# Kernel optimization log

Measured on AMD Instinct MI355X. Metric: run time of the kernel, lower is better.

Reference implementation:

```python
import jax, jax.numpy as jnp
import numpy as np

TOKEN_SELF_ATTN_VALUE = -50000.0
EPS_NORM = 1e-12
EPS_SCATTER = 1e-5
COMMITMENT = 1e-4


def _l2norm(x):
    return x / jnp.maximum(jnp.linalg.norm(x, axis=-1, keepdims=True), EPS_NORM)


def _shift(x):
    # relative-position shift, faithful to the torch `shift` helper
    # x: [..., i, j] -> [..., i, j]
    *pre, i, j = x.shape
    x = jnp.concatenate([x, jnp.zeros((*pre, i, i), x.dtype)], axis=-1)  # [..., i, i+j]
    l = i + j - 1
    x = x.reshape(*pre, i * (i + j))
    pad = (-x.shape[-1]) % l
    x = jnp.concatenate([x, jnp.zeros((*pre, pad), x.dtype)], axis=-1)
    x = x.reshape(*pre, -1, l)
    return x[..., :i, i - 1:]


def setup_inputs() -> dict:
    key = jax.random.key(0)
    k1, k2, k3, k4 = jax.random.split(key, 4)
    b, h, t, d = 4, 8, 8192, 64
    c, wsz = 64, 128
    qk = jax.random.normal(k1, (b, h, t, d), jnp.float32)
    v = jax.random.normal(k2, (b, h, t, d), jnp.float32)
    means = jax.random.normal(k3, (h, c, d), jnp.float32)
    means = _l2norm(means)  # trained kmeans means are unit-normalized
    rel_w = jax.random.normal(k4, (wsz, h, d), jnp.float32) * 0.02
    return {"qk": qk, "v": v, "means": means, "rel_w": rel_w}


def reference(qk, v, means, rel_w):
    b, h, t, d = qk.shape
    c = means.shape[1]
    wsz = min(rel_w.shape[0], t)

    # ---- kmeans routing (eval path: no iterations, fixed means) ----
    k_routing = _l2norm(qk)                                   # [b,h,t,d]
    dists = jnp.einsum('bhld,hcd->bhlc', k_routing, means)    # cosine sims
    buckets = jnp.argmax(dists, axis=-1)                      # [b,h,t]
    # top-wsz tokens per cluster, sorted ascending (matches topk -> sort -> transpose)
    _, idx = jax.lax.top_k(jnp.swapaxes(dists, -1, -2), wsz)  # [b,h,c,wsz]
    indices = jnp.sort(idx, axis=-1).reshape(b, h, c * wsz)   # [b,h,c*wsz]

    # commitment loss against routed means (means is a non-trainable buffer)
    routed_means = means[jnp.arange(h)[None, :, None], buckets]  # [b,h,t,d]
    loss = jnp.mean((k_routing - routed_means) ** 2) * COMMITMENT

    # ---- gather routed windows ----
    qk_g = jnp.take_along_axis(qk, indices[..., None], axis=2).reshape(b, h, c, wsz, d)
    v_g = jnp.take_along_axis(v, indices[..., None], axis=2).reshape(b, h, c, wsz, d)
    q = qk_g
    k = _l2norm(qk_g)

    scale = d ** -0.5
    dots = jnp.einsum('bhnid,bhnjd->bhnij', q, k) * scale     # [b,h,c,wsz,wsz]
    rel = jnp.einsum('bhnid,jhd->bhnij', q, rel_w) * scale
    dots = dots + _shift(rel)

    # token cannot attend to itself within its window
    eye = jnp.eye(wsz, dtype=bool)
    dots = jnp.where(eye, TOKEN_SELF_ATTN_VALUE, dots)

    attn = jax.nn.softmax(dots, axis=-1)
    bo = jnp.einsum('bhnij,bhnjd->bhnid', attn, v_g).reshape(b, h, c * wsz, d)

    # ---- scatter-mean back to original token positions ----
    def scat(idx1, src1):  # idx1: [N], src1: [N,d]
        num = jnp.zeros((t, d), src1.dtype).at[idx1].add(src1)
        den = jnp.zeros((t, d), src1.dtype).at[idx1].add(jnp.ones_like(src1))
        return num / (den + EPS_SCATTER)

    out = jax.vmap(jax.vmap(scat))(indices, bo)               # [b,h,t,d]
    return out, loss
```

## Files before the change

kernel.cpp:

```cpp
#include <hip/hip_runtime.h>
#include <hip/hip_bf16.h>
#include <math.h>

#define NB 4
#define NH 8
#define TT 8192
#define DD 64
#define NC 64
#define WW 128
#define BHN 32
#define SCALE 0.125f
#define INVCAP 24
#define TPB 128

typedef __bf16  bf16x8 __attribute__((ext_vector_type(8)));
typedef float   f32x4  __attribute__((ext_vector_type(4)));
typedef double  f64x4  __attribute__((ext_vector_type(4)));
typedef unsigned long long u64;

#define MFMA(a, b, c) __builtin_amdgcn_mfma_f32_16x16x32_bf16((a), (b), (c), 0, 0, 0)

__device__ __forceinline__ u64 fixkey(double dv) {
    double k = (dv + 1.0) * 4611686018427387904.0;
    k = fmin(fmax(k, 0.0), 9223371487098961920.0);
    return (u64)k;
}

__global__ __launch_bounds__(256) void k_dists(
    const float* __restrict__ qk, const float* __restrict__ means,
    u64* __restrict__ keys, double* __restrict__ lossa)
{
    __shared__ float  qS[TPB * 66];
    __shared__ float  mS[NC * 65];
    __shared__ double invS[TPB];
    __shared__ double s2S[TPB];
    __shared__ double mn2[NC];
    __shared__ double red[4];

    const int bh  = blockIdx.x;
    const int h   = bh & 7;
    const int tid = threadIdx.x;
    const int t0  = blockIdx.y * TPB;

    {
        const float* mp = means + h * (NC * DD);
        for (int i = tid; i < NC * DD; i += 256)
            mS[(i >> 6) * 65 + (i & 63)] = mp[i];
    }
    {
        const float4* src = (const float4*)(qk + ((size_t)bh * TT + t0) * DD);
        for (int i = tid; i < TPB * DD / 4; i += 256) {
            const float4 v = src[i];
            float* dst = qS + (i >> 4) * 66 + (i & 15) * 4;
            *(float2*)(dst)     = make_float2(v.x, v.y);
            *(float2*)(dst + 2) = make_float2(v.z, v.w);
        }
    }
    __syncthreads();

    if (tid < NC) {
        double s = 0.0;
        const float* rp = mS + tid * 65;
        for (int d = 0; d < DD; d++) { const double m = (double)rp[d]; s = fma(m, m, s); }
        mn2[tid] = s;
    }
    if (tid < TPB) {
        double s = 0.0;
        const float* rp = qS + tid * 66;
#pragma unroll
        for (int d = 0; d < DD; d += 2) {
            const float2 f = *(const float2*)(rp + d);
            s = fma((double)f.x, (double)f.x, s);
            s = fma((double)f.y, (double)f.y, s);
        }
        const double inv = 1.0 / fmax(sqrt(s), 1e-12);
        invS[tid] = inv;
        s2S[tid]  = s * inv * inv;
    }
    __syncthreads();

    const int lane = tid & 63;
    const int wv   = tid >> 6;
    const int lo   = lane & 15;
    const int quad = lane >> 4;

    double lt_lane = 0.0;

#pragma unroll
    for (int tt = 0; tt < 2; tt++) {
        const int tloc = (wv * 2 + tt) * 16 + lo;
        double Bf[16];
#pragma unroll
        for (int s = 0; s < 16; s++)
            Bf[s] = (double)qS[tloc * 66 + quad + 4 * s];
        const double inv = invS[tloc];

        double rawmax = -1.0e300; int cbest = 0;
        u64* kout = keys + (size_t)bh * NC * TT + (t0 + tloc);

#pragma unroll
        for (int ct = 0; ct < 4; ct++) {
            f64x4 acc = (f64x4){0.0, 0.0, 0.0, 0.0};
#pragma unroll
            for (int s = 0; s < 16; s++) {
                const double Af = (double)mS[(ct * 16 + lo) * 65 + quad + 4 * s];
                acc = __builtin_amdgcn_mfma_f64_16x16x4f64(Af, Bf[s], acc, 0, 0, 0);
            }
#pragma unroll
            for (int r = 0; r < 4; r++) {
                const double raw = acc[r];
                const int c = ct * 16 + quad * 4 + r;
                if (raw > rawmax) { rawmax = raw; cbest = c; }
                kout[(size_t)c * TT] = fixkey(raw * inv);
            }
        }

#pragma unroll
        for (int off = 16; off < 64; off <<= 1) {
            const double ov = __shfl_xor(rawmax, off);
            const int    oc = __shfl_xor(cbest, off);
            if (ov > rawmax || (ov == rawmax && oc < cbest)) { rawmax = ov; cbest = oc; }
        }
        if (quad == 0)
            lt_lane += s2S[tloc] + mn2[cbest] - 2.0 * rawmax * inv;
    }

#pragma unroll
    for (int o = 32; o; o >>= 1) lt_lane += __shfl_xor(lt_lane, o);
    if (lane == 0) red[wv] = lt_lane;
    __syncthreads();
    if (tid == 0) atomicAdd(lossa, red[0] + red[1] + red[2] + red[3]);
}

__global__ __launch_bounds__(256) void k_topk(
    const u64* __restrict__ keys, int* __restrict__ indices,
    unsigned int* __restrict__ cnt, unsigned short* __restrict__ inv)
{
    __shared__ unsigned int hist[4][256];
    __shared__ int wsum[8];
    __shared__ int bc_bin, bc_rank, bc_cnt;

    const int bhc = blockIdx.x, tid = threadIdx.x;
    const int wv = tid >> 6, lane = tid & 63;
    const int bh = bhc >> 6;

    u64 key[32];
    {
        const ulonglong2* p = (const ulonglong2*)(keys + (size_t)bhc * TT + tid * 32);
#pragma unroll
        for (int i = 0; i < 16; i++) { ulonglong2 u = p[i]; key[2*i] = u.x; key[2*i+1] = u.y; }
    }

    u64 thr = 0;
    int need = 128, gshift = 55, prevShift = 0;
    unsigned int* hb = &hist[0][0];

    for (int level = 0; level < 8; level++) {
        const int shift = (level < 7) ? (55 - 8 * level) : 0;
        hb[tid] = 0; hb[tid + 256] = 0; hb[tid + 512] = 0; hb[tid + 768] = 0;
        __syncthreads();
        unsigned int* hw = hist[wv];
        if (level == 0) {
#pragma unroll
            for (int i = 0; i < 32; i++)
                atomicAdd(&hw[(unsigned int)(key[i] >> 55)], 1u);
        } else {
            const u64 pv = thr >> prevShift;
#pragma unroll
            for (int i = 0; i < 32; i++)
                if ((key[i] >> prevShift) == pv)
                    atomicAdd(&hw[(unsigned int)(key[i] >> shift) & 255u], 1u);
        }
        __syncthreads();

        const int b = 255 - tid;
        const int c = hist[0][b] + hist[1][b] + hist[2][b] + hist[3][b];
        int incl = c;
#pragma unroll
        for (int o = 1; o < 64; o <<= 1) {
            const int v = __shfl_up(incl, o);
            if (lane >= o) incl += v;
        }
        if (lane == 63) wsum[wv] = incl;
        __syncthreads();
        int above = incl - c;
        for (int wj = 0; wj < wv; wj++) above += wsum[wj];
        if (above < need && above + c >= need) {
            bc_bin = b; bc_rank = above; bc_cnt = c;
        }
        __syncthreads();
        thr |= ((u64)(unsigned int)bc_bin) << shift;
        need -= bc_rank;
        gshift = shift;
        prevShift = shift;
        if (bc_cnt == need || shift == 0) break;
    }

    const u64 tg = thr >> gshift;
    int cgt = 0, ceq = 0;
#pragma unroll
    for (int i = 0; i < 32; i++) {
        const u64 kg = key[i] >> gshift;
        cgt += (kg > tg) ? 1 : 0;
        ceq += (kg == tg) ? 1 : 0;
    }
    int ig = cgt, ie = ceq;
#pragma unroll
    for (int o = 1; o < 64; o <<= 1) {
        const int vg = __shfl_up(ig, o);
        const int ve = __shfl_up(ie, o);
        if (lane >= o) { ig += vg; ie += ve; }
    }
    if (lane == 63) { wsum[wv] = ig; wsum[4 + wv] = ie; }
    __syncthreads();
    int pgt = ig - cgt, peq = ie - ceq;
    for (int wj = 0; wj < wv; wj++) { pgt += wsum[wj]; peq += wsum[4 + wj]; }

    const int rneed = need;
    int* outp = indices + bhc * WW;
    unsigned int* cntb = cnt + (bh << 13);
    unsigned short* invb = inv + (((size_t)bh << 13) * INVCAP);
    const int cbase = (bhc & 63) * WW;
    int g = 0, e = 0;
#pragma unroll
    for (int i = 0; i < 32; i++) {
        const int tok = tid * 32 + i;
        const u64 kg = key[i] >> gshift;
        if (kg > tg) {
            const int tb = (peq + e < rneed) ? (peq + e) : rneed;
            const int wpos = pgt + g + tb;
            outp[wpos] = tok;
            const unsigned int pos = atomicAdd(&cntb[tok], 1u);
            if (pos < INVCAP) invb[(size_t)tok * INVCAP + pos] = (unsigned short)(cbase + wpos);
            g++;
        } else if (kg == tg) {
            if (peq + e < rneed) {
                const int wpos = pgt + g + peq + e;
                outp[wpos] = tok;
                const unsigned int pos = atomicAdd(&cntb[tok], 1u);
                if (pos < INVCAP) invb[(size_t)tok * INVCAP + pos] = (unsigned short)(cbase + wpos);
            }
            e++;
        }
    }
}

#define QS_ADDR(row, gi) (((row) << 6) + ((((gi) ^ ((row) & 7))) << 3))

__global__ __launch_bounds__(512) void k_attn(
    const float* __restrict__ qk, const float* __restrict__ vin,
    const float* __restrict__ rel_w, const int* __restrict__ indices,
    float* __restrict__ bo)
{
    __shared__ __attribute__((aligned(16))) __bf16 uv[64 * 136];
    __shared__ __attribute__((aligned(16))) __bf16 rs[128 * 136];
    __shared__ float invs[128];
    __shared__ int   idxs[128];

    const int tid  = threadIdx.x;
    const int lane = tid & 63;
    const int wv   = tid >> 6;
    const int lo   = lane & 15;
    const int quad = lane >> 4;
    const int rbase = wv * 16;

    const int bhc = blockIdx.x;
    const int bh  = bhc >> 6;
    const int h   = bh & 7;

    if (tid < 128) idxs[tid] = indices[bhc * WW + tid];
    __syncthreads();

    const int r  = tid >> 2;
    const int qp = tid & 3;
    const size_t rowoff = ((size_t)bh * TT + idxs[r]) * DD + qp * 16;
    float4 q0, q1, q2, q3, vreg[4];
    {
        const float4* qsrc = (const float4*)(qk + rowoff);
        q0 = qsrc[0]; q1 = qsrc[1]; q2 = qsrc[2]; q3 = qsrc[3];
        const float4* vsrc = (const float4*)(vin + rowoff);
        vreg[0] = vsrc[0]; vreg[1] = vsrc[1]; vreg[2] = vsrc[2]; vreg[3] = vsrc[3];
    }
    {
        float ssq = q0.x*q0.x + q0.y*q0.y + q0.z*q0.z + q0.w*q0.w
                  + q1.x*q1.x + q1.y*q1.y + q1.z*q1.z + q1.w*q1.w
                  + q2.x*q2.x + q2.y*q2.y + q2.z*q2.z + q2.w*q2.w
                  + q3.x*q3.x + q3.y*q3.y + q3.z*q3.z + q3.w*q3.w;
        ssq += __shfl_xor(ssq, 1);
        ssq += __shfl_xor(ssq, 2);
        if (qp == 0) invs[r] = 1.0f / fmaxf(sqrtf(ssq), 1e-12f);
        bf16x8 va, vb;
        va[0]=(__bf16)q0.x; va[1]=(__bf16)q0.y; va[2]=(__bf16)q0.z; va[3]=(__bf16)q0.w;
        va[4]=(__bf16)q1.x; va[5]=(__bf16)q1.y; va[6]=(__bf16)q1.z; va[7]=(__bf16)q1.w;
        vb[0]=(__bf16)q2.x; vb[1]=(__bf16)q2.y; vb[2]=(__bf16)q2.z; vb[3]=(__bf16)q2.w;
        vb[4]=(__bf16)q3.x; vb[5]=(__bf16)q3.y; vb[6]=(__bf16)q3.z; vb[7]=(__bf16)q3.w;
        *(bf16x8*)(uv + QS_ADDR(r, qp * 2))     = va;
        *(bf16x8*)(uv + QS_ADDR(r, qp * 2 + 1)) = vb;
    }
    __syncthreads();

    f32x4 acc[8];

#pragma unroll
    for (int nt = 0; nt < 8; nt++) acc[nt] = (f32x4){0.f, 0.f, 0.f, 0.f};
#pragma unroll
    for (int k0 = 0; k0 < 64; k0 += 32) {
        bf16x8 qa = *(const bf16x8*)(uv + QS_ADDR(rbase + lo, (k0 >> 3) + quad));
#pragma unroll
        for (int nt = 0; nt < 8; nt++) {
            const float* wp = rel_w + (size_t)((nt * 16 + lo) * 8 + h) * 64 + k0 + quad * 8;
            float4 w0 = ((const float4*)wp)[0];
            float4 w1 = ((const float4*)wp)[1];
            bf16x8 wb;
            wb[0]=(__bf16)w0.x; wb[1]=(__bf16)w0.y; wb[2]=(__bf16)w0.z; wb[3]=(__bf16)w0.w;
            wb[4]=(__bf16)w1.x; wb[5]=(__bf16)w1.y; wb[6]=(__bf16)w1.z; wb[7]=(__bf16)w1.w;
            acc[nt] = MFMA(qa, wb, acc[nt]);
        }
    }
#pragma unroll
    for (int nt = 0; nt < 8; nt++)
#pragma unroll
        for (int rg = 0; rg < 4; rg++)
            rs[(rbase + quad * 4 + rg) * 136 + nt * 16 + lo] = (__bf16)acc[nt][rg];

#pragma unroll
    for (int nt = 0; nt < 8; nt++) acc[nt] = (f32x4){0.f, 0.f, 0.f, 0.f};
#pragma unroll
    for (int k0 = 0; k0 < 64; k0 += 32) {
        bf16x8 qa = *(const bf16x8*)(uv + QS_ADDR(rbase + lo, (k0 >> 3) + quad));
#pragma unroll
        for (int nt = 0; nt < 8; nt++) {
            bf16x8 qb = *(const bf16x8*)(uv + QS_ADDR(nt * 16 + lo, (k0 >> 3) + quad));
            acc[nt] = MFMA(qa, qb, acc[nt]);
        }
    }

    float inv_j[8];
#pragma unroll
    for (int nt = 0; nt < 8; nt++) inv_j[nt] = invs[nt * 16 + lo];

#pragma unroll
    for (int rg = 0; rg < 4; rg++) {
        const int i = rbase + quad * 4 + rg;
#pragma unroll
        for (int nt = 0; nt < 8; nt++) {
            const int j = nt * 16 + lo;
            float val = acc[nt][rg] * inv_j[nt] * SCALE;
            if (j <= i) val += SCALE * (float)rs[i * 136 + (j + 127 - i)];
            if (j == i) val = -50000.0f;
            acc[nt][rg] = val;
        }
    }

#pragma unroll
    for (int rg = 0; rg < 4; rg++) {
        float m = -3.0e38f;
#pragma unroll
        for (int nt = 0; nt < 8; nt++) m = fmaxf(m, acc[nt][rg]);
#pragma unroll
        for (int msk = 1; msk < 16; msk <<= 1) m = fmaxf(m, __shfl_xor(m, msk));
        float s = 0.f;
#pragma unroll
        for (int nt = 0; nt < 8; nt++) {
            const float e = __expf(acc[nt][rg] - m);
            acc[nt][rg] = e; s += e;
        }
#pragma unroll
        for (int msk = 1; msk < 16; msk <<= 1) s += __shfl_xor(s, msk);
        const float is = 1.0f / s;
        const int i = rbase + quad * 4 + rg;
#pragma unroll
        for (int nt = 0; nt < 8; nt++)
            rs[i * 136 + nt * 16 + lo] = (__bf16)(acc[nt][rg] * is);
    }
    __syncthreads();

    __bf16* vt = uv;
#pragma unroll
    for (int i = 0; i < 4; i++) {
        vt[(qp * 16 + 4*i + 0) * 136 + r] = (__bf16)vreg[i].x;
        vt[(qp * 16 + 4*i + 1) * 136 + r] = (__bf16)vreg[i].y;
        vt[(qp * 16 + 4*i + 2) * 136 + r] = (__bf16)vreg[i].z;
        vt[(qp * 16 + 4*i + 3) * 136 + r] = (__bf16)vreg[i].w;
    }
    __syncthreads();

    f32x4 accO[4];
#pragma unroll
    for (int nt = 0; nt < 4; nt++) accO[nt] = (f32x4){0.f, 0.f, 0.f, 0.f};
#pragma unroll
    for (int k0 = 0; k0 < 128; k0 += 32) {
        bf16x8 pa = *(const bf16x8*)(rs + (rbase + lo) * 136 + k0 + quad * 8);
#pragma unroll
        for (int nt = 0; nt < 4; nt++) {
            bf16x8 vb = *(const bf16x8*)(vt + (nt * 16 + lo) * 136 + k0 + quad * 8);
            accO[nt] = MFMA(pa, vb, accO[nt]);
        }
    }

    float* bb = bo + (size_t)bhc * (WW * DD);
#pragma unroll
    for (int rg = 0; rg < 4; rg++) {
        const int i = rbase + quad * 4 + rg;
#pragma unroll
        for (int nt = 0; nt < 4; nt++)
            bb[(size_t)i * DD + nt * 16 + lo] = accO[nt][rg];
    }
}

__global__ __launch_bounds__(256) void k_out(
    const float* __restrict__ bo, const unsigned int* __restrict__ cnt,
    const unsigned short* __restrict__ inv, const double* __restrict__ lossa,
    float* __restrict__ out)
{
    const int tid = threadIdx.x;
    const int g = blockIdx.x * 16 + (tid >> 4);
    const int l = tid & 15;
    const int bh = g >> 13;
    const unsigned int n = cnt[g];
    const int nc = (n < (unsigned)INVCAP) ? (int)n : INVCAP;
    const unsigned short* ip = inv + (size_t)g * INVCAP;
    const float* bbase = bo + (((size_t)bh << 13) * DD);
    float4 s = {0.f, 0.f, 0.f, 0.f};
    for (int e = 0; e < nc; e++) {
        const int slot = ip[e];
        float4 v4 = *(const float4*)(bbase + (size_t)slot * DD + l * 4);
        s.x += v4.x; s.y += v4.y; s.z += v4.z; s.w += v4.w;
    }
    const float r = 1.0f / ((float)n + 1e-5f);
    s.x *= r; s.y *= r; s.z *= r; s.w *= r;
    *(float4*)(out + (size_t)g * DD + l * 4) = s;
    if (g == 0 && l == 0) out[16777216] = (float)(lossa[0] * (0.0001 / 16777216.0));
}

extern "C" void kernel_launch(void* const* d_in, const int* in_sizes, int n_in,
                              void* d_out, int out_size, void* d_ws, size_t ws_size,
                              hipStream_t stream) {
    (void)in_sizes; (void)n_in; (void)ws_size; (void)out_size;
    const float* qk    = (const float*)d_in[0];
    const float* v     = (const float*)d_in[1];
    const float* means = (const float*)d_in[2];
    const float* rel_w = (const float*)d_in[3];
    float* out = (float*)d_out;

    char* ws = (char*)d_ws;
    const size_t KEYS_B = (size_t)BHN * NC * TT * 8;
    const size_t IDX_B  = (size_t)BHN * NC * WW * 4;
    const size_t CNT_B  = (size_t)BHN * TT * 4;
    u64*            keys  = (u64*)ws;
    float*          bo    = (float*)ws;
    int*            idx   = (int*)(ws + KEYS_B);
    unsigned int*   cnt   = (unsigned int*)(ws + KEYS_B + IDX_B);
    double*         lossa = (double*)(ws + KEYS_B + IDX_B + CNT_B);
    unsigned short* inv   = (unsigned short*)(ws + KEYS_B + IDX_B + CNT_B + 4096);

    hipMemsetAsync(ws + KEYS_B + IDX_B, 0, CNT_B + 4096, stream);

    k_dists<<<dim3(BHN, TT / TPB), 256, 0, stream>>>(qk, means, keys, lossa);
    k_topk<<<BHN * NC, 256, 0, stream>>>(keys, idx, cnt, inv);
    k_attn<<<BHN * NC, 512, 0, stream>>>(qk, v, rel_w, idx, bo);
    k_out<<<BHN * TT / 16, 256, 0, stream>>>(bo, cnt, inv, lossa, out);
}
```

Before: 388.5 us.

## Shrink top-k sort keys to 32-bit and pre-convert rel_w to bf16

The distance keys written by k_dists and read by k_topk shrink from 64-bit to 32-bit fixed-point. This halves the largest intermediate buffer's traffic and cuts the radix-select from up to eight levels to four. A small prep kernel converts rel_w to bf16 once, so k_attn loads packed bf16 directly instead of converting floats per block, and k_attn reads its row index straight from global memory rather than staging indices in shared memory. The 32-bit keys lose resolution, so near-tied cosine similarities may pick different top-k members or a different order than the 64-bit version.

Measured after the change: 344.8 us. -11.2%, faster.

```diff
diff --git a/kernel.cpp b/kernel.cpp
--- a/kernel.cpp
+++ b/kernel.cpp
@@ -14,21 +14,33 @@
 #define TPB 128
 
 typedef __bf16  bf16x8 __attribute__((ext_vector_type(8)));
+typedef __bf16  bf16x4 __attribute__((ext_vector_type(4)));
 typedef float   f32x4  __attribute__((ext_vector_type(4)));
 typedef double  f64x4  __attribute__((ext_vector_type(4)));
 typedef unsigned long long u64;
+typedef unsigned int u32;
 
 #define MFMA(a, b, c) __builtin_amdgcn_mfma_f32_16x16x32_bf16((a), (b), (c), 0, 0, 0)
 
-__device__ __forceinline__ u64 fixkey(double dv) {
-    double k = (dv + 1.0) * 4611686018427387904.0;
-    k = fmin(fmax(k, 0.0), 9223371487098961920.0);
-    return (u64)k;
+__device__ __forceinline__ u32 fixkey32(double dv) {
+    double k = (dv + 1.0) * 2147483648.0;
+    k = fmin(fmax(k, 0.0), 4294967295.0);
+    return (u32)k;
+}
+
+__global__ __launch_bounds__(256) void k_prep(
+    const float* __restrict__ rel_w, __bf16* __restrict__ relb)
+{
+    const int i = blockIdx.x * 256 + threadIdx.x;
+    const float4 v = ((const float4*)rel_w)[i];
+    bf16x4 o;
+    o[0] = (__bf16)v.x; o[1] = (__bf16)v.y; o[2] = (__bf16)v.z; o[3] = (__bf16)v.w;
+    *(bf16x4*)(relb + i * 4) = o;
 }
 
 __global__ __launch_bounds__(256) void k_dists(
     const float* __restrict__ qk, const float* __restrict__ means,
-    u64* __restrict__ keys, double* __restrict__ lossa)
+    u32* __restrict__ keys, double* __restrict__ lossa)
 {
     __shared__ float  qS[TPB * 66];
     __shared__ float  mS[NC * 65];
@@ -96,7 +108,7 @@
         const double inv = invS[tloc];
 
         double rawmax = -1.0e300; int cbest = 0;
-        u64* kout = keys + (size_t)bh * NC * TT + (t0 + tloc);
+        u32* kout = keys + (size_t)bh * NC * TT + (t0 + tloc);
 
 #pragma unroll
         for (int ct = 0; ct < 4; ct++) {
@@ -111,7 +123,7 @@
                 const double raw = acc[r];
                 const int c = ct * 16 + quad * 4 + r;
                 if (raw > rawmax) { rawmax = raw; cbest = c; }
-                kout[(size_t)c * TT] = fixkey(raw * inv);
+                kout[(size_t)c * TT] = fixkey32(raw * inv);
             }
         }
 
@@ -133,7 +145,7 @@
 }
 
 __global__ __launch_bounds__(256) void k_topk(
-    const u64* __restrict__ keys, int* __restrict__ indices,
+    const u32* __restrict__ keys, int* __restrict__ indices,
     unsigned int* __restrict__ cnt, unsigned short* __restrict__ inv)
 {
     __shared__ unsigned int hist[4][256];
@@ -144,32 +156,35 @@
     const int wv = tid >> 6, lane = tid & 63;
     const int bh = bhc >> 6;
 
-    u64 key[32];
+    u32 key[32];
     {
-        const ulonglong2* p = (const ulonglong2*)(keys + (size_t)bhc * TT + tid * 32);
-#pragma unroll
-        for (int i = 0; i < 16; i++) { ulonglong2 u = p[i]; key[2*i] = u.x; key[2*i+1] = u.y; }
-    }
-
-    u64 thr = 0;
-    int need = 128, gshift = 55, prevShift = 0;
+        const uint4* p = (const uint4*)(keys + (size_t)bhc * TT + tid * 32);
+#pragma unroll
+        for (int i = 0; i < 8; i++) {
+            uint4 u = p[i];
+            key[4*i] = u.x; key[4*i+1] = u.y; key[4*i+2] = u.z; key[4*i+3] = u.w;
+        }
+    }
+
+    u32 thr = 0;
+    int need = 128, gshift = 24, prevShift = 0;
     unsigned int* hb = &hist[0][0];
 
-    for (int level = 0; level < 8; level++) {
-        const int shift = (level < 7) ? (55 - 8 * level) : 0;
+    for (int level = 0; level < 4; level++) {
+        const int shift = 24 - 8 * level;
         hb[tid] = 0; hb[tid + 256] = 0; hb[tid + 512] = 0; hb[tid + 768] = 0;
         __syncthreads();
         unsigned int* hw = hist[wv];
         if (level == 0) {
 #pragma unroll
             for (int i = 0; i < 32; i++)
-                atomicAdd(&hw[(unsigned int)(key[i] >> 55)], 1u);
+                atomicAdd(&hw[key[i] >> 24], 1u);
         } else {
-            const u64 pv = thr >> prevShift;
+            const u32 pv = thr >> prevShift;
 #pragma unroll
             for (int i = 0; i < 32; i++)
                 if ((key[i] >> prevShift) == pv)
-                    atomicAdd(&hw[(unsigned int)(key[i] >> shift) & 255u], 1u);
+                    atomicAdd(&hw[(key[i] >> shift) & 255u], 1u);
         }
         __syncthreads();
 
@@ -189,18 +204,18 @@
             bc_bin = b; bc_rank = above; bc_cnt = c;
         }
         __syncthreads();
-        thr |= ((u64)(unsigned int)bc_bin) << shift;
+        thr |= ((u32)bc_bin) << shift;
         need -= bc_rank;
         gshift = shift;
         prevShift = shift;
         if (bc_cnt == need || shift == 0) break;
     }
 
-    const u64 tg = thr >> gshift;
+    const u32 tg = thr >> gshift;
     int cgt = 0, ceq = 0;
 #pragma unroll
     for (int i = 0; i < 32; i++) {
-        const u64 kg = key[i] >> gshift;
+        const u32 kg = key[i] >> gshift;
         cgt += (kg > tg) ? 1 : 0;
         ceq += (kg == tg) ? 1 : 0;
     }
@@ -225,7 +240,7 @@
 #pragma unroll
     for (int i = 0; i < 32; i++) {
         const int tok = tid * 32 + i;
-        const u64 kg = key[i] >> gshift;
+        const u32 kg = key[i] >> gshift;
         if (kg > tg) {
             const int tb = (peq + e < rneed) ? (peq + e) : rneed;
             const int wpos = pgt + g + tb;
@@ -249,13 +264,12 @@
 
 __global__ __launch_bounds__(512) void k_attn(
     const float* __restrict__ qk, const float* __restrict__ vin,
-    const float* __restrict__ rel_w, const int* __restrict__ indices,
+    const __bf16* __restrict__ relb, const int* __restrict__ indices,
     float* __restrict__ bo)
 {
     __shared__ __attribute__((aligned(16))) __bf16 uv[64 * 136];
     __shared__ __attribute__((aligned(16))) __bf16 rs[128 * 136];
     __shared__ float invs[128];
-    __shared__ int   idxs[128];
 
     const int tid  = threadIdx.x;
     const int lane = tid & 63;
@@ -268,12 +282,10 @@
     const int bh  = bhc >> 6;
     const int h   = bh & 7;
 
-    if (tid < 128) idxs[tid] = indices[bhc * WW + tid];
-    __syncthreads();
-
     const int r  = tid >> 2;
     const int qp = tid & 3;
-    const size_t rowoff = ((size_t)bh * TT + idxs[r]) * DD + qp * 16;
+    const int rowidx = indices[bhc * WW + r];
+    const size_t rowoff = ((size_t)bh * TT + rowidx) * DD + qp * 16;
     float4 q0, q1, q2, q3, vreg[4];
     {
         const float4* qsrc = (const float4*)(qk + rowoff);
@@ -308,12 +320,7 @@
         bf16x8 qa = *(const bf16x8*)(uv + QS_ADDR(rbase + lo, (k0 >> 3) + quad));
 #pragma unroll
         for (int nt = 0; nt < 8; nt++) {
-            const float* wp = rel_w + (size_t)((nt * 16 + lo) * 8 + h) * 64 + k0 + quad * 8;
-            float4 w0 = ((const float4*)wp)[0];
-            float4 w1 = ((const float4*)wp)[1];
-            bf16x8 wb;
-            wb[0]=(__bf16)w0.x; wb[1]=(__bf16)w0.y; wb[2]=(__bf16)w0.z; wb[3]=(__bf16)w0.w;
-            wb[4]=(__bf16)w1.x; wb[5]=(__bf16)w1.y; wb[6]=(__bf16)w1.z; wb[7]=(__bf16)w1.w;
+            const bf16x8 wb = *(const bf16x8*)(relb + ((nt * 16 + lo) * 8 + h) * 64 + k0 + quad * 8);
             acc[nt] = MFMA(qa, wb, acc[nt]);
         }
     }
@@ -444,20 +451,23 @@
     float* out = (float*)d_out;
 
     char* ws = (char*)d_ws;
-    const size_t KEYS_B = (size_t)BHN * NC * TT * 8;
+    const size_t KEYS_B = (size_t)BHN * NC * TT * 4;
     const size_t IDX_B  = (size_t)BHN * NC * WW * 4;
     const size_t CNT_B  = (size_t)BHN * TT * 4;
-    u64*            keys  = (u64*)ws;
+    const size_t INV_B  = (size_t)BHN * TT * INVCAP * 2;
+    u32*            keys  = (u32*)ws;
     float*          bo    = (float*)ws;
     int*            idx   = (int*)(ws + KEYS_B);
     unsigned int*   cnt   = (unsigned int*)(ws + KEYS_B + IDX_B);
     double*         lossa = (double*)(ws + KEYS_B + IDX_B + CNT_B);
     unsigned short* inv   = (unsigned short*)(ws + KEYS_B + IDX_B + CNT_B + 4096);
+    __bf16*         relb  = (__bf16*)(ws + KEYS_B + IDX_B + CNT_B + 4096 + INV_B);
 
     hipMemsetAsync(ws + KEYS_B + IDX_B, 0, CNT_B + 4096, stream);
 
+    k_prep<<<64, 256, 0, stream>>>(rel_w, relb);
     k_dists<<<dim3(BHN, TT / TPB), 256, 0, stream>>>(qk, means, keys, lossa);
     k_topk<<<BHN * NC, 256, 0, stream>>>(keys, idx, cnt, inv);
-    k_attn<<<BHN * NC, 512, 0, stream>>>(qk, v, rel_w, idx, bo);
+    k_attn<<<BHN * NC, 512, 0, stream>>>(qk, v, relb, idx, bo);
     k_out<<<BHN * TT / 16, 256, 0, stream>>>(bo, cnt, inv, lossa, out);
 }
```
